# Optimization experiments

Hardware: AMD Instinct MI355X
Metric: run time of the kernel (lower is better)

The kernel has to match this reference:

```python
import jax, jax.numpy as jnp
import numpy as np

NUM_HEADS = 16
ROPE_THETA = 10000.0


def _vision_rope_tables(seq_len, head_dim):
    # Llama4 vision ('mllama4') 2D rotary: x/y patch-grid positions,
    # interleaved (non-neox) complex pairs. Returns cos/sin [S, head_dim//2].
    idx = int(np.sqrt(seq_len))  # patches per side (24 for 336/14)
    pos = np.arange(seq_len)
    fx = (pos % idx + 1).astype(np.float32)
    fy = (pos // idx + 1).astype(np.float32)
    freq_dim = head_dim // 2
    rope_freq = 1.0 / ROPE_THETA ** (
        np.arange(0, freq_dim, 2)[: freq_dim // 2].astype(np.float32) / freq_dim
    )
    fx = np.repeat(fx[:, None] * rope_freq[None, :], 2, axis=-1)  # [S, freq_dim]
    fy = np.repeat(fy[:, None] * rope_freq[None, :], 2, axis=-1)
    freqs = np.concatenate([fx, fy], axis=-1)[:, ::2]  # [S, head_dim//2]
    return jnp.asarray(np.cos(freqs)), jnp.asarray(np.sin(freqs))


def _apply_rope(x, cos, sin):
    # x: [B, S, H, D]; even/odd interleaved pairs treated as complex numbers
    B, S, H, D = x.shape
    xr = x.reshape(B, S, H, D // 2, 2)
    x0, x1 = xr[..., 0], xr[..., 1]
    c = cos[None, :, None, :]
    s = sin[None, :, None, :]
    o0 = x0 * c - x1 * s
    o1 = x0 * s + x1 * c
    return jnp.stack([o0, o1], axis=-1).reshape(B, S, H, D)


def setup_inputs() -> dict:
    key = jax.random.key(0)
    ks = jax.random.split(key, 5)
    E = 1408
    B, S = 16, 576
    scale = 0.02
    return {
        "hidden_states": jax.random.normal(ks[0], (B, S, E), dtype=jnp.float32),
        "w_qkv": jax.random.normal(ks[1], (E, 3 * E), dtype=jnp.float32) * scale,
        "b_qkv": jax.random.normal(ks[2], (3 * E,), dtype=jnp.float32) * scale,
        "w_o": jax.random.normal(ks[3], (E, E), dtype=jnp.float32) * scale,
        "b_o": jax.random.normal(ks[4], (E,), dtype=jnp.float32) * scale,
    }


def reference(hidden_states, w_qkv, b_qkv, w_o, b_o):
    B, S, E = hidden_states.shape
    H = NUM_HEADS
    D = E // H
    scaling = D ** -0.5

    qkv = hidden_states @ w_qkv + b_qkv  # [B,S,3E]
    q, k, v = jnp.split(qkv, 3, axis=-1)
    q = q.reshape(B, S, H, D)
    k = k.reshape(B, S, H, D)
    v = v.reshape(B, S, H, D)

    cos, sin = _vision_rope_tables(S, D)
    q = _apply_rope(q, cos, sin)
    k = _apply_rope(k, cos, sin)

    q = q * scaling
    scores = jnp.einsum("bqhd,bkhd->bhqk", q, k)  # full bidirectional attention
    probs = jax.nn.softmax(scores, axis=-1)
    attn = jnp.einsum("bhqk,bkhd->bqhd", probs, v).reshape(B, S, E)

    return attn @ w_o + b_o
```

## Files before the change

kernel.cpp:

```cpp
#include <hip/hip_runtime.h>
#include <hip/hip_bf16.h>


typedef unsigned short UST;
typedef __attribute__((ext_vector_type(8))) __bf16 bf16x8;
typedef __attribute__((ext_vector_type(4))) float f32x4;
typedef __attribute__((ext_vector_type(8))) UST us8;
typedef __attribute__((ext_vector_type(4))) UST us4;

typedef __attribute__((address_space(3))) unsigned int lds_u32;
typedef const __attribute__((address_space(1))) unsigned int glob_u32;

static __device__ __forceinline__ float bf2f(UST u){
  unsigned int x = ((unsigned int)u) << 16;
  return __builtin_bit_cast(float, x);
}
static __device__ __forceinline__ UST f2bf(float f){
  unsigned int x = __builtin_bit_cast(unsigned int, f);
  x += 0x7fffu + ((x >> 16) & 1u);
  return (UST)(x >> 16);
}

__global__ void k_tables(float* __restrict__ cosT, float* __restrict__ sinT){
  int s = blockIdx.x;
  int d = threadIdx.x;
  if (d >= 88) return;
  int p = d >> 1;
  int tt = p % 22;
  double comp = (p < 22) ? (double)(s % 24 + 1) : (double)(s / 24 + 1);
  double a = comp * pow(10000.0, -(double)tt / 22.0);
  cosT[d*576 + s] = (float)cos(a);
  sinT[d*576 + s] = (float)sin(a);
}

__global__ void k_zero(UST* __restrict__ qa, UST* __restrict__ ka, UST* __restrict__ vt){
  int c = blockIdx.x*256 + threadIdx.x;
  int bh = c / 576, s = c - bh*576;
  us8 z = {0,0,0,0,0,0,0,0};
  *(us8*)(qa + ((size_t)bh*576 + s)*96 + 88) = z;
  *(us8*)(ka + ((size_t)bh*576 + s)*96 + 88) = z;
  *(us8*)(vt + (size_t)bh*55296 + 50688 + s*8) = z;
}

__global__ void k_cvt(const float* __restrict__ in, UST* __restrict__ out, int n4){
  int i = blockIdx.x * 256 + threadIdx.x;
  if (i >= n4) return;
  float4 v = ((const float4*)in)[i];
  us4 o; o[0]=f2bf(v.x); o[1]=f2bf(v.y); o[2]=f2bf(v.z); o[3]=f2bf(v.w);
  *(us4*)(out + 4*(size_t)i) = o;
}

__global__ void k_cvt_t(const float* __restrict__ W, UST* __restrict__ Bt, int K, int N){
  __shared__ __align__(16) UST tl[64][70];
  int kt = blockIdx.x, nt = blockIdx.y;
  int t = threadIdx.x;
  int k = t >> 2, u = t & 3;
  const float* src = W + (size_t)(kt*64 + k)*N + nt*64 + u*16;
#pragma unroll
  for (int i = 0; i < 4; ++i){
    float4 v = *(const float4*)(src + 4*i);
    UST* d = &tl[k][u*16 + 4*i];
    d[0]=f2bf(v.x); d[1]=f2bf(v.y); d[2]=f2bf(v.z); d[3]=f2bf(v.w);
  }
  __syncthreads();
  int n = t >> 2;
  UST* dst = Bt + (size_t)(nt*64 + n)*K + kt*64 + u*16;
#pragma unroll
  for (int i = 0; i < 2; ++i){
    us8 o;
#pragma unroll
    for (int j = 0; j < 8; ++j) o[j] = tl[u*16 + 8*i + j][n];
    *(us8*)(dst + 8*i) = o;
  }
}

template<int EPI>
__global__ __launch_bounds__(256, 2) void k_gemm(
    const UST* __restrict__ A, const UST* __restrict__ Bt,
    const float* __restrict__ bias, void* __restrict__ Cout,
    int M, int N, int K,
    UST* __restrict__ qa, UST* __restrict__ ka, UST* __restrict__ vt,
    const float* __restrict__ cosT, const float* __restrict__ sinT)
{
  __shared__ __align__(16) UST lA[2][128][64];
  __shared__ __align__(16) UST lB[2][128][64];
  const int t = threadIdx.x;
  const int bm = blockIdx.x, bn = blockIdx.y;
  const int wave = t >> 6, lane = t & 63;
  const int lm = lane & 15, g = lane >> 4;
  const int wr = (wave >> 1) << 6, wc = (wave & 1) << 6;
  const int lrow = lane >> 3;
  const int lcol = (((lane & 7) ^ lrow) << 3);
  const UST* Ag = A  + (size_t)(bm*128 + wave*32 + lrow)*K + lcol;
  const UST* Bg = Bt + (size_t)(bn*128 + wave*32 + lrow)*K + lcol;

  f32x4 zero = {0.f,0.f,0.f,0.f};
  f32x4 acc[4][4];
#pragma unroll
  for (int i=0;i<4;++i)
#pragma unroll
    for (int j=0;j<4;++j) acc[i][j] = zero;

  const int nkt = K >> 6;
  auto stage = [&](int kt, int buf){
#pragma unroll
    for (int c = 0; c < 4; ++c){
      __builtin_amdgcn_global_load_lds((glob_u32*)(Ag + (size_t)kt*64 + (size_t)(8*c)*K),
                                       (lds_u32*)(&lA[buf][wave*32 + 8*c][0]), 16, 0, 0);
      __builtin_amdgcn_global_load_lds((glob_u32*)(Bg + (size_t)kt*64 + (size_t)(8*c)*K),
                                       (lds_u32*)(&lB[buf][wave*32 + 8*c][0]), 16, 0, 0);
    }
  };

  stage(0, 0);
  __syncthreads();
  const int swz = (lm & 7) << 3;

  for (int kt = 0; kt < nkt; ++kt){
    const int cur = kt & 1;
    if (kt + 1 < nkt) stage(kt + 1, cur ^ 1);
#pragma unroll
    for (int ks = 0; ks < 2; ++ks){
      bf16x8 af[4], bfv[4];
      const int cb = (ks*32 + g*8) ^ swz;
#pragma unroll
      for (int mf = 0; mf < 4; ++mf)
        af[mf] = __builtin_bit_cast(bf16x8, *(const us8*)&lA[cur][wr + mf*16 + lm][cb]);
#pragma unroll
      for (int nf = 0; nf < 4; ++nf)
        bfv[nf] = __builtin_bit_cast(bf16x8, *(const us8*)&lB[cur][wc + nf*16 + lm][cb]);
#pragma unroll
      for (int mf = 0; mf < 4; ++mf)
#pragma unroll
        for (int nf = 0; nf < 4; ++nf)
          acc[mf][nf] = __builtin_amdgcn_mfma_f32_16x16x32_bf16(af[mf], bfv[nf], acc[mf][nf], 0, 0, 0);
    }
    __syncthreads();
  }

  if (EPI == 0){
#pragma unroll
    for (int nf = 0; nf < 4; ++nf){
      const int col = bn*128 + wc + nf*16 + lm;
      const float bv = bias[col];
#pragma unroll
      for (int mf = 0; mf < 4; ++mf){
        const size_t rb = (size_t)(bm*128 + wr + mf*16 + g*4);
#pragma unroll
        for (int r = 0; r < 4; ++r)
          ((float*)Cout)[(rb + r)*(size_t)N + col] = acc[mf][nf][r] + bv;
      }
    }
  } else {
    const int j = bn / 11;
    const int bnr = bn - j*11;
    if (j == 2){
#pragma unroll
      for (int nf = 0; nf < 4; ++nf){
        const int cv = bnr*128 + wc + nf*16 + lm;
        const float bv = bias[2816 + cv];
        const int h = cv / 88, d = cv - h*88;
#pragma unroll
        for (int mf = 0; mf < 4; ++mf){
          const int rb = bm*128 + wr + mf*16 + g*4;
          const int b2 = rb / 576, s = rb - b2*576;
          UST* dst = vt + ((size_t)((b2*16 + h)*96 + d))*576 + s;
          us4 pk;
#pragma unroll
          for (int r = 0; r < 4; ++r) pk[r] = f2bf(acc[mf][nf][r] + bv);
          *(us4*)dst = pk;
        }
      }
    } else {
      UST* outp = j ? ka : qa;
      const float sc = j ? 1.0f : 0.10660035817780521f;
      const bool even = (lm & 1) == 0;
#pragma unroll
      for (int nf = 0; nf < 4; ++nf){
        const int cv = bnr*128 + wc + nf*16 + lm;
        const float bv = bias[j*1408 + cv];
        const int h = cv / 88, d = cv - h*88;
        const float* cT = cosT + d*576;
        const float* sT = sinT + d*576;
#pragma unroll
        for (int mf = 0; mf < 4; ++mf){
          const int rb = bm*128 + wr + mf*16 + g*4;
          const int b2 = rb / 576, s = rb - b2*576;
          float4 c4 = *(const float4*)(cT + s);
          float4 s4 = *(const float4*)(sT + s);
          float cc[4] = {c4.x, c4.y, c4.z, c4.w};
          float ss[4] = {s4.x, s4.y, s4.z, s4.w};
          UST* dst = outp + ((size_t)(b2*16 + h)*576 + s)*96 + d;
#pragma unroll
          for (int r = 0; r < 4; ++r){
            float vs = acc[mf][nf][r] + bv;
            float vo = __shfl_xor(vs, 1, 64);
            float o = even ? (vs*cc[r] - vo*ss[r])
                           : (vo*ss[r] + vs*cc[r]);
            dst[(size_t)r*96] = f2bf(o * sc);
          }
        }
      }
    }
  }
}

__global__ __launch_bounds__(256, 2) void k_attn(
    const UST* __restrict__ qa, const UST* __restrict__ ka,
    const UST* __restrict__ vt, UST* __restrict__ outp)
{
  __shared__ __align__(16) UST lK[64][104];
  __shared__ __align__(16) UST lV[96][72];
  __shared__ __align__(16) UST lP[4][16][72];
  const int bh = blockIdx.x, qt = blockIdx.y;
  const int t = threadIdx.x, wave = t >> 6, lane = t & 63;
  const int lm = lane & 15, g = lane >> 4;
  const int h = bh & 15, b = bh >> 4;

  bf16x8 qf[3];
  {
    const UST* qp = qa + ((size_t)bh*576 + qt*64 + wave*16 + lm)*96 + g*8;
#pragma unroll
    for (int ks = 0; ks < 3; ++ks) qf[ks] = __builtin_bit_cast(bf16x8, *(const us8*)(qp + ks*32));
  }
  f32x4 zero = {0.f,0.f,0.f,0.f};
  f32x4 acc[6];
#pragma unroll
  for (int i = 0; i < 6; ++i) acc[i] = zero;
  float psum[4];
#pragma unroll
  for (int r = 0; r < 4; ++r) psum[r] = 0.f;

  const UST* kbase = ka + (size_t)bh*576*96;
  const UST* vbase = vt + (size_t)bh*96*576;

  for (int kvt = 0; kvt < 9; ++kvt){
    {
      int r = t >> 2, u = t & 3;
      const UST* src = kbase + (size_t)(kvt*64 + r)*96 + u*24;
#pragma unroll
      for (int i = 0; i < 3; ++i)
        *(uint4*)&lK[r][u*24 + i*8] = *(const uint4*)(src + i*8);
    }
    if (t < 192){
      int d = t >> 1, hf = t & 1;
      const UST* src = vbase + (size_t)d*576 + kvt*64 + hf*32;
#pragma unroll
      for (int i = 0; i < 4; ++i)
        *(uint4*)&lV[d][hf*32 + i*8] = *(const uint4*)(src + i*8);
    }
    __syncthreads();

    f32x4 sc[4];
#pragma unroll
    for (int i = 0; i < 4; ++i) sc[i] = zero;
    __builtin_amdgcn_s_setprio(1);
#pragma unroll
    for (int ks = 0; ks < 3; ++ks){
#pragma unroll
      for (int nf = 0; nf < 4; ++nf){
        bf16x8 kf = __builtin_bit_cast(bf16x8, *(const us8*)&lK[nf*16 + lm][ks*32 + g*8]);
        sc[nf] = __builtin_amdgcn_mfma_f32_16x16x32_bf16(qf[ks], kf, sc[nf], 0, 0, 0);
      }
    }
    __builtin_amdgcn_s_setprio(0);

#pragma unroll
    for (int r = 0; r < 4; ++r){
      float ls = 0.f;
#pragma unroll
      for (int nf = 0; nf < 4; ++nf){
        float p = __expf(sc[nf][r]);
        sc[nf][r] = p;
        ls += p;
      }
      psum[r] += ls;
    }

#pragma unroll
    for (int nf = 0; nf < 4; ++nf)
#pragma unroll
      for (int r = 0; r < 4; ++r)
        lP[wave][4*g + r][nf*16 + lm] = f2bf(sc[nf][r]);

    bf16x8 pa[2];
#pragma unroll
    for (int ks2 = 0; ks2 < 2; ++ks2)
      pa[ks2] = __builtin_bit_cast(bf16x8, *(const us8*)&lP[wave][lm][ks2*32 + g*8]);
    __builtin_amdgcn_s_setprio(1);
#pragma unroll
    for (int ks2 = 0; ks2 < 2; ++ks2)
#pragma unroll
      for (int df = 0; df < 6; ++df){
        bf16x8 vf = __builtin_bit_cast(bf16x8, *(const us8*)&lV[df*16 + lm][ks2*32 + g*8]);
        acc[df] = __builtin_amdgcn_mfma_f32_16x16x32_bf16(pa[ks2], vf, acc[df], 0, 0, 0);
      }
    __builtin_amdgcn_s_setprio(0);
    __syncthreads();
  }

#pragma unroll
  for (int m = 1; m <= 8; m <<= 1)
#pragma unroll
    for (int r = 0; r < 4; ++r) psum[r] += __shfl_xor(psum[r], m, 64);
  float inv[4];
#pragma unroll
  for (int r = 0; r < 4; ++r) inv[r] = 1.f / psum[r];

  const size_t rowt = (size_t)b*576 + qt*64 + wave*16;
#pragma unroll
  for (int df = 0; df < 6; ++df){
    int d = df*16 + lm;
    if (d < 88){
#pragma unroll
      for (int r = 0; r < 4; ++r)
        outp[(rowt + 4*g + r)*1408 + h*88 + d] = f2bf(acc[df][r] * inv[r]);
    }
  }
}

extern "C" void kernel_launch(void* const* d_in, const int* in_sizes, int n_in,
                              void* d_out, int out_size, void* d_ws, size_t ws_size,
                              hipStream_t stream)
{
  (void)in_sizes; (void)n_in; (void)out_size; (void)ws_size;
  const float* hs   = (const float*)d_in[0];
  const float* wqkv = (const float*)d_in[1];
  const float* bqkv = (const float*)d_in[2];
  const float* wo   = (const float*)d_in[3];
  const float* bo   = (const float*)d_in[4];
  float* out = (float*)d_out;

  char* w = (char*)d_ws;
  UST* A_bf   = (UST*)(w);
  UST* Bt1    = (UST*)(w + 25952256);
  UST* Bt2    = (UST*)(w + 37847040);
  UST* qa     = (UST*)(w + 41811968);
  UST* ka     = (UST*)(w + 70123520);
  UST* vt     = (UST*)(w + 98435072);
  float* cosT = (float*)(w + 126746624);
  float* sinT = (float*)(w + 126949376);

  k_tables<<<576, 128, 0, stream>>>(cosT, sinT);
  k_zero<<<576, 256, 0, stream>>>(qa, ka, vt);
  k_cvt<<<12672, 256, 0, stream>>>(hs, A_bf, 3244032);
  k_cvt_t<<<dim3(22, 66), 256, 0, stream>>>(wqkv, Bt1, 1408, 4224);
  k_cvt_t<<<dim3(22, 22), 256, 0, stream>>>(wo, Bt2, 1408, 1408);
  k_gemm<3><<<dim3(72, 33), 256, 0, stream>>>(A_bf, Bt1, bqkv, nullptr, 9216, 4224, 1408,
                                              qa, ka, vt, cosT, sinT);
  k_attn<<<dim3(256, 9), 256, 0, stream>>>(qa, ka, vt, A_bf);
  k_gemm<0><<<dim3(72, 11), 256, 0, stream>>>(A_bf, Bt2, bo, out, 9216, 1408, 1408,
                                              nullptr, nullptr, nullptr, nullptr, nullptr);
}
```

Measured before the change: 307.8 us.

## Stage QKV GEMM epilogue through LDS for vectorized RoPE and V-transpose stores

The QKV GEMM epilogue now writes the bias-added accumulators into a swizzled 64KB LDS buffer that aliases the A/B tiles. It then reads them back so each thread emits 16-byte bf16x8 stores for Q/K (with RoPE applied on local pairs, no shuffles) and for the transposed V layout. This replaces scattered 2-byte and 8-byte stores. The cos/sin tables are also interleaved per position into a single array so each thread fetches them with two float4 loads. The cost is an extra LDS round-trip and a barrier in the epilogue.

```diff
diff --git a/kernel.cpp b/kernel.cpp
--- a/kernel.cpp
+++ b/kernel.cpp
@@ -21,16 +21,15 @@
   return (UST)(x >> 16);
 }
 
-__global__ void k_tables(float* __restrict__ cosT, float* __restrict__ sinT){
+__global__ void k_tables(float* __restrict__ cs2){
   int s = blockIdx.x;
-  int d = threadIdx.x;
-  if (d >= 88) return;
-  int p = d >> 1;
+  int p = threadIdx.x;
+  if (p >= 44) return;
   int tt = p % 22;
   double comp = (p < 22) ? (double)(s % 24 + 1) : (double)(s / 24 + 1);
   double a = comp * pow(10000.0, -(double)tt / 22.0);
-  cosT[d*576 + s] = (float)cos(a);
-  sinT[d*576 + s] = (float)sin(a);
+  cs2[s*88 + 2*p]     = (float)cos(a);
+  cs2[s*88 + 2*p + 1] = (float)sin(a);
 }
 
 __global__ void k_zero(UST* __restrict__ qa, UST* __restrict__ ka, UST* __restrict__ vt){
@@ -80,10 +79,13 @@
     const float* __restrict__ bias, void* __restrict__ Cout,
     int M, int N, int K,
     UST* __restrict__ qa, UST* __restrict__ ka, UST* __restrict__ vt,
-    const float* __restrict__ cosT, const float* __restrict__ sinT)
+    const float* __restrict__ cs2)
 {
-  __shared__ __align__(16) UST lA[2][128][64];
-  __shared__ __align__(16) UST lB[2][128][64];
+  __shared__ __align__(16) char SMEM[65536];
+  UST (*lA)[128][64] = reinterpret_cast<UST(*)[128][64]>(SMEM);
+  UST (*lB)[128][64] = reinterpret_cast<UST(*)[128][64]>(SMEM + 32768);
+  float* sm = reinterpret_cast<float*>(SMEM);
+
   const int t = threadIdx.x;
   const int bm = blockIdx.x, bn = blockIdx.y;
   const int wave = t >> 6, lane = t & 63;
@@ -152,54 +154,70 @@
       }
     }
   } else {
+#pragma unroll
+    for (int nf = 0; nf < 4; ++nf){
+      const int col = wc + nf*16 + lm;
+      const float bv = bias[bn*128 + col];
+#pragma unroll
+      for (int mf = 0; mf < 4; ++mf){
+#pragma unroll
+        for (int r = 0; r < 4; ++r){
+          const int row = wr + mf*16 + g*4 + r;
+          const int colS = (((col >> 3) ^ (row & 7)) << 3) | (col & 7);
+          sm[row*128 + colS] = acc[mf][nf][r] + bv;
+        }
+      }
+    }
+    __syncthreads();
+
     const int j = bn / 11;
     const int bnr = bn - j*11;
     if (j == 2){
 #pragma unroll
-      for (int nf = 0; nf < 4; ++nf){
-        const int cv = bnr*128 + wc + nf*16 + lm;
-        const float bv = bias[2816 + cv];
-        const int h = cv / 88, d = cv - h*88;
-#pragma unroll
-        for (int mf = 0; mf < 4; ++mf){
-          const int rb = bm*128 + wr + mf*16 + g*4;
-          const int b2 = rb / 576, s = rb - b2*576;
-          UST* dst = vt + ((size_t)((b2*16 + h)*96 + d))*576 + s;
-          us4 pk;
-#pragma unroll
-          for (int r = 0; r < 4; ++r) pk[r] = f2bf(acc[mf][nf][r] + bv);
-          *(us4*)dst = pk;
+      for (int i = 0; i < 8; ++i){
+        const int idx = t + 256*i;
+        const int col = idx & 127, rch = idx >> 7;
+        const int cv = bnr*128 + col;
+        const int h = cv / 88, dv = cv - h*88;
+        const int s0g = bm*128 + rch*8;
+        const int b2 = s0g / 576, sl = s0g - b2*576;
+        us8 o;
+#pragma unroll
+        for (int k = 0; k < 8; ++k){
+          const int row = rch*8 + k;
+          const int colS = (((col >> 3) ^ (row & 7)) << 3) | (col & 7);
+          o[k] = f2bf(sm[row*128 + colS]);
         }
+        *(us8*)(vt + ((size_t)(b2*16 + h)*96 + dv)*576 + sl) = o;
       }
     } else {
       UST* outp = j ? ka : qa;
       const float sc = j ? 1.0f : 0.10660035817780521f;
-      const bool even = (lm & 1) == 0;
-#pragma unroll
-      for (int nf = 0; nf < 4; ++nf){
-        const int cv = bnr*128 + wc + nf*16 + lm;
-        const float bv = bias[j*1408 + cv];
-        const int h = cv / 88, d = cv - h*88;
-        const float* cT = cosT + d*576;
-        const float* sT = sinT + d*576;
-#pragma unroll
-        for (int mf = 0; mf < 4; ++mf){
-          const int rb = bm*128 + wr + mf*16 + g*4;
-          const int b2 = rb / 576, s = rb - b2*576;
-          float4 c4 = *(const float4*)(cT + s);
-          float4 s4 = *(const float4*)(sT + s);
-          float cc[4] = {c4.x, c4.y, c4.z, c4.w};
-          float ss[4] = {s4.x, s4.y, s4.z, s4.w};
-          UST* dst = outp + ((size_t)(b2*16 + h)*576 + s)*96 + d;
-#pragma unroll
-          for (int r = 0; r < 4; ++r){
-            float vs = acc[mf][nf][r] + bv;
-            float vo = __shfl_xor(vs, 1, 64);
-            float o = even ? (vs*cc[r] - vo*ss[r])
-                           : (vo*ss[r] + vs*cc[r]);
-            dst[(size_t)r*96] = f2bf(o * sc);
-          }
+#pragma unroll
+      for (int i = 0; i < 8; ++i){
+        const int idx = t + 256*i;
+        const int ch = idx & 15, rr = idx >> 4;
+        const int cv = bnr*128 + ch*8;
+        const int h = cv / 88, d0 = cv - h*88;
+        const int rb = bm*128 + rr;
+        const int b2 = rb / 576, s = rb - b2*576;
+        const float* src = &sm[rr*128 + ((ch ^ (rr & 7)) << 3)];
+        float x[8];
+#pragma unroll
+        for (int k = 0; k < 8; ++k) x[k] = src[k];
+        const float* tb = cs2 + s*88 + d0;
+        float4 q0 = *(const float4*)(tb);
+        float4 q1 = *(const float4*)(tb + 4);
+        float cc[4]  = {q0.x, q0.z, q1.x, q1.z};
+        float ssv[4] = {q0.y, q0.w, q1.y, q1.w};
+        us8 o;
+#pragma unroll
+        for (int p = 0; p < 4; ++p){
+          float o0 = (x[2*p]*cc[p]  - x[2*p+1]*ssv[p]) * sc;
+          float o1 = (x[2*p]*ssv[p] + x[2*p+1]*cc[p])  * sc;
+          o[2*p] = f2bf(o0); o[2*p+1] = f2bf(o1);
         }
+        *(us8*)(outp + ((size_t)(b2*16 + h)*576 + s)*96 + d0) = o;
       }
     }
   }
@@ -338,17 +356,16 @@
   UST* qa     = (UST*)(w + 41811968);
   UST* ka     = (UST*)(w + 70123520);
   UST* vt     = (UST*)(w + 98435072);
-  float* cosT = (float*)(w + 126746624);
-  float* sinT = (float*)(w + 126949376);
-
-  k_tables<<<576, 128, 0, stream>>>(cosT, sinT);
+  float* cs2  = (float*)(w + 126746624);
+
+  k_tables<<<576, 64, 0, stream>>>(cs2);
   k_zero<<<576, 256, 0, stream>>>(qa, ka, vt);
   k_cvt<<<12672, 256, 0, stream>>>(hs, A_bf, 3244032);
   k_cvt_t<<<dim3(22, 66), 256, 0, stream>>>(wqkv, Bt1, 1408, 4224);
   k_cvt_t<<<dim3(22, 22), 256, 0, stream>>>(wo, Bt2, 1408, 1408);
   k_gemm<3><<<dim3(72, 33), 256, 0, stream>>>(A_bf, Bt1, bqkv, nullptr, 9216, 4224, 1408,
-                                              qa, ka, vt, cosT, sinT);
+                                              qa, ka, vt, cs2);
   k_attn<<<dim3(256, 9), 256, 0, stream>>>(qa, ka, vt, A_bf);
   k_gemm<0><<<dim3(72, 11), 256, 0, stream>>>(A_bf, Bt2, bo, out, 9216, 1408, 1408,
-                                              nullptr, nullptr, nullptr, nullptr, nullptr);
-}
+                                              nullptr, nullptr, nullptr, nullptr);
+}
```

Measured after the change: 293.0 us. 4.8% less time.
